# Optimization experiments

Hardware: AMD Instinct MI355X
Metric: run time of the kernel (lower is better)

Reference implementation:

```python
import jax, jax.numpy as jnp
import numpy as np

N_NODES = 100000


def setup_inputs() -> dict:
    key = jax.random.key(0)
    ks = jax.random.split(key, 9)
    x = jax.random.normal(ks[0], (N_NODES, 500), dtype=jnp.float32)
    # lin1: Linear(m=500, hidden=64, bias=False) -> weight [hidden, m]
    W1 = jax.random.normal(ks[1], (64, 500), dtype=jnp.float32) * 0.02
    # lin_final: Linear(3*hidden=192, m_y=10, bias=False) -> weight [m_y, 3*hidden]
    Wf = jax.random.normal(ks[2], (10, 192), dtype=jnp.float32) * 0.02
    # 1-hop normalized adjacency in COO form (600k nnz)
    src1 = jax.random.randint(ks[3], (600000,), 0, N_NODES, dtype=jnp.int32)
    dst1 = jax.random.randint(ks[4], (600000,), 0, N_NODES, dtype=jnp.int32)
    val1 = jax.random.uniform(ks[5], (600000,), dtype=jnp.float32)
    # 2-hop normalized adjacency in COO form (1.2M nnz)
    src2 = jax.random.randint(ks[6], (1200000,), 0, N_NODES, dtype=jnp.int32)
    dst2 = jax.random.randint(ks[7], (1200000,), 0, N_NODES, dtype=jnp.int32)
    val2 = jax.random.uniform(ks[8], (1200000,), dtype=jnp.float32)
    return {"x": x, "W1": W1, "Wf": Wf,
            "src1": src1, "dst1": dst1, "val1": val1,
            "src2": src2, "dst2": dst2, "val2": val2}


def _spmm(src, dst, val, h):
    # sparse.mm(A, h): out[dst] += val * h[src]
    return jax.ops.segment_sum(val[:, None] * h[src], dst, num_segments=N_NODES)


def reference(x, W1, Wf, src1, dst1, val1, src2, dst2, val2):
    h = jax.nn.relu(x @ W1.T)                 # [N, hidden]
    h1 = _spmm(src1, dst1, val1, h)           # [N, hidden]
    h2 = _spmm(src2, dst2, val2, h)           # [N, hidden]
    h_final = jnp.concatenate([h, h1, h2], axis=1)  # [N, 3*hidden]
    # dropout is identity in eval mode
    return h_final @ Wf.T                     # [N, m_y]
```

## Files before the change

### kernel.cpp

```cpp
#include <hip/hip_runtime.h>
#include <hip/hip_bf16.h>

#define NN   100000
#define KD   500
#define KP   512
#define HID  64
#define LWS  264
#define GS   24

typedef short frag8 __attribute__((ext_vector_type(8)));
typedef float f32x4 __attribute__((ext_vector_type(4)));

static __device__ __forceinline__ unsigned short f2b(float f) {
    return __builtin_bit_cast(unsigned short, __float2bfloat16(f));
}

__global__ __launch_bounds__(256) void k0_w1bf(const float* __restrict__ W1,
                                               unsigned short* __restrict__ W1bf)
{
    const int i = blockIdx.x * 256 + threadIdx.x;
    const int c = i >> 9;
    const int k = i & 511;
    const float v = (k < KD) ? W1[c * KD + k] : 0.f;
    W1bf[i] = f2b(v);
}

__global__ __launch_bounds__(256, 4) void k1_mfma(const float* __restrict__ x,
                                                  const unsigned short* __restrict__ W1bf,
                                                  float* __restrict__ h, int n)
{
    __shared__ unsigned short lw[64 * LWS];
    const int tid   = threadIdx.x;
    const int lane  = tid & 63;
    const int wid   = tid >> 6;
    const int l15   = lane & 15;
    const int l4    = lane >> 4;
    const int koffl = 8 * l4;

    const long rowBlk = (long)blockIdx.x * 64;
    long ra = rowBlk + wid * 16 + l15;
    if (ra >= n) ra = n - 1;
    const float* xp = x + ra * KD + koffl;

    f32x4 acc[4] = {};
    const float4 z = make_float4(0.f, 0.f, 0.f, 0.f);

    for (int c = 0; c < 2; ++c) {
        if (c) __syncthreads();
        #pragma unroll
        for (int it = 0; it < 8; ++it) {
            const int idx = tid + it * 256;
            const int r   = idx >> 5;
            const int q   = idx & 31;
            *(uint4*)&lw[r * LWS + q * 8] =
                *(const uint4*)&W1bf[r * KP + c * 256 + q * 8];
        }
        __syncthreads();

        int k0 = c * 256;
        float4 lo = (k0 + koffl     < KD) ? *(const float4*)(xp + k0)     : z;
        float4 hi = (k0 + koffl + 4 < KD) ? *(const float4*)(xp + k0 + 4) : z;

        #pragma unroll
        for (int ks = 0; ks < 8; ++ks) {
            float4 nlo = z, nhi = z;
            if (ks < 7) {
                const int kn = c * 256 + (ks + 1) * 32;
                nlo = (kn + koffl     < KD) ? *(const float4*)(xp + kn)     : z;
                nhi = (kn + koffl + 4 < KD) ? *(const float4*)(xp + kn + 4) : z;
            }
            frag8 a;
            a[0]=f2b(lo.x); a[1]=f2b(lo.y); a[2]=f2b(lo.z); a[3]=f2b(lo.w);
            a[4]=f2b(hi.x); a[5]=f2b(hi.y); a[6]=f2b(hi.z); a[7]=f2b(hi.w);
            const int koffw = ks * 32 + koffl;
            #pragma unroll
            for (int g = 0; g < 4; ++g) {
                const frag8 b = *(const frag8*)&lw[(g * 16 + l15) * LWS + koffw];
                acc[g] = __builtin_amdgcn_mfma_f32_16x16x32_bf16(a, b, acc[g], 0, 0, 0);
            }
            lo = nlo; hi = nhi;
        }
    }

    #pragma unroll
    for (int r = 0; r < 4; ++r) {
        const long row = rowBlk + wid * 16 + l4 * 4 + r;
        if (row < n) {
            #pragma unroll
            for (int g = 0; g < 4; ++g)
                h[row * HID + g * 16 + l15] = fmaxf(acc[g][r], 0.f);
        }
    }
}

__global__ __launch_bounds__(256) void k2_proj(const float* __restrict__ h,
                                               const float* __restrict__ Wf,
                                               float* __restrict__ out,
                                               float* __restrict__ g, int n)
{
    __shared__ float lwf[10 * 196];
    const int tid = threadIdx.x;
    for (int idx = tid; idx < 480; idx += 256) {
        const int j = idx / 48;
        const int q = idx - j * 48;
        const float4 v = *(const float4*)&Wf[j * 192 + 4 * q];
        *(float4*)&lwf[j * 196 + 4 * q] = v;
    }
    __syncthreads();

    const long row = (long)blockIdx.x * 8 + (tid >> 5);
    const int  j   = tid & 31;
    if (row < n && j < 30) {
        const int wrow = (j < 10) ? j : ((j < 20) ? j - 10 : j - 20);
        const int coff = (j < 10) ? 0 : ((j < 20) ? 64 : 128);
        const float* wp = &lwf[wrow * 196 + coff];
        const float* hp = &h[row * HID];
        float s = 0.f;
        #pragma unroll
        for (int q = 0; q < 16; ++q) {
            const float4 hv = *(const float4*)&hp[4 * q];
            const float4 wv = *(const float4*)&wp[4 * q];
            s += hv.x * wv.x + hv.y * wv.y + hv.z * wv.z + hv.w * wv.w;
        }
        if (j < 10)      out[row * 10 + j] = s;
        else if (j < 20) g[row * GS + (j - 10)] = s;
        else             g[row * GS + 12 + (j - 20)] = s;
    }
}

__global__ __launch_bounds__(256) void k_scatter(const int* __restrict__ src1,
                                                 const int* __restrict__ dst1,
                                                 const float* __restrict__ val1, int n1,
                                                 const int* __restrict__ src2,
                                                 const int* __restrict__ dst2,
                                                 const float* __restrict__ val2, int nt,
                                                 const float* __restrict__ g,
                                                 float* __restrict__ out)
{
    const int stride = gridDim.x * 256;
    for (int t0 = blockIdx.x * 256 + threadIdx.x; t0 < nt; t0 += 4 * stride) {
        float contrib[4];
        int   oidx[4];
        #pragma unroll
        for (int u = 0; u < 4; ++u) {
            const int tu = t0 + u * stride;
            oidx[u] = -1;
            contrib[u] = 0.f;
            if (tu < nt) {
                const bool h1 = tu < n1;
                const int  tt = h1 ? tu : tu - n1;
                const int  e  = (int)((unsigned)tt / 10u);
                const int  j  = tt - 10 * e;
                const int* sp = h1 ? src1 : src2;
                const int* dp = h1 ? dst1 : dst2;
                const float* vp = h1 ? val1 : val2;
                const int   s = sp[e];
                const int   d = dp[e];
                const float v = vp[e];
                contrib[u] = v * g[(size_t)s * GS + (h1 ? 0 : 12) + j];
                oidx[u] = d * 10 + j;
            }
        }
        #pragma unroll
        for (int u = 0; u < 4; ++u)
            if (oidx[u] >= 0) unsafeAtomicAdd(&out[oidx[u]], contrib[u]);
    }
}

extern "C" void kernel_launch(void* const* d_in, const int* in_sizes, int n_in,
                              void* d_out, int out_size, void* d_ws, size_t ws_size,
                              hipStream_t stream)
{
    const float* x    = (const float*)d_in[0];
    const float* W1   = (const float*)d_in[1];
    const float* Wf   = (const float*)d_in[2];
    const int*   src1 = (const int*)d_in[3];
    const int*   dst1 = (const int*)d_in[4];
    const float* val1 = (const float*)d_in[5];
    const int*   src2 = (const int*)d_in[6];
    const int*   dst2 = (const int*)d_in[7];
    const float* val2 = (const float*)d_in[8];
    const int nnz1 = in_sizes[3];
    const int nnz2 = in_sizes[6];
    const int n = NN;

    unsigned short* W1bf = (unsigned short*)d_ws;
    float* h   = (float*)((char*)d_ws + 64 * KP * 2);
    float* g   = h + (size_t)NN * HID;
    float* out = (float*)d_out;

    k0_w1bf<<<128, 256, 0, stream>>>(W1, W1bf);
    k1_mfma<<<(n + 63) / 64, 256, 0, stream>>>(x, W1bf, h, n);
    k2_proj<<<(n + 7) / 8, 256, 0, stream>>>(h, Wf, out, g, n);
    const int n1 = 10 * nnz1;
    const int nt = n1 + 10 * nnz2;
    int nb = (nt + 1023) / 1024;
    if (nb > 2048) nb = 2048;
    k_scatter<<<nb, 256, 0, stream>>>(src1, dst1, val1, n1,
                                      src2, dst2, val2, nt, g, out);
}
```

Before: 231.9 us.

## Privatize scatter atomics per XCD into replicated buffers, then reduce

Result: slower. 250.1 us (+7.8%).

```diff
diff --git a/kernel.cpp b/kernel.cpp
--- a/kernel.cpp
+++ b/kernel.cpp
@@ -7,6 +7,7 @@
 #define HID  64
 #define LWS  264
 #define GS   24
+#define NXCD 8
 
 typedef short frag8 __attribute__((ext_vector_type(8)));
 typedef float f32x4 __attribute__((ext_vector_type(4)));
@@ -128,43 +129,70 @@
     }
 }
 
-__global__ __launch_bounds__(256) void k_scatter(const int* __restrict__ src1,
-                                                 const int* __restrict__ dst1,
-                                                 const float* __restrict__ val1, int n1,
-                                                 const int* __restrict__ src2,
-                                                 const int* __restrict__ dst2,
-                                                 const float* __restrict__ val2, int nt,
-                                                 const float* __restrict__ g,
-                                                 float* __restrict__ out)
-{
-    const int stride = gridDim.x * 256;
-    for (int t0 = blockIdx.x * 256 + threadIdx.x; t0 < nt; t0 += 4 * stride) {
-        float contrib[4];
-        int   oidx[4];
-        #pragma unroll
-        for (int u = 0; u < 4; ++u) {
-            const int tu = t0 + u * stride;
-            oidx[u] = -1;
-            contrib[u] = 0.f;
-            if (tu < nt) {
-                const bool h1 = tu < n1;
-                const int  tt = h1 ? tu : tu - n1;
-                const int  e  = (int)((unsigned)tt / 10u);
-                const int  j  = tt - 10 * e;
-                const int* sp = h1 ? src1 : src2;
-                const int* dp = h1 ? dst1 : dst2;
-                const float* vp = h1 ? val1 : val2;
-                const int   s = sp[e];
-                const int   d = dp[e];
-                const float v = vp[e];
-                contrib[u] = v * g[(size_t)s * GS + (h1 ? 0 : 12) + j];
-                oidx[u] = d * 10 + j;
-            }
-        }
-        #pragma unroll
-        for (int u = 0; u < 4; ++u)
-            if (oidx[u] >= 0) unsafeAtomicAdd(&out[oidx[u]], contrib[u]);
-    }
+__global__ __launch_bounds__(256) void k_scatter_rep(const int* __restrict__ src1,
+                                                     const int* __restrict__ dst1,
+                                                     const float* __restrict__ val1, int n1,
+                                                     const int* __restrict__ src2,
+                                                     const int* __restrict__ dst2,
+                                                     const float* __restrict__ val2, int nt,
+                                                     const float* __restrict__ g,
+                                                     float* __restrict__ rep)
+{
+    const int t = blockIdx.x * 256 + threadIdx.x;
+    if (t >= nt) return;
+    const bool h1 = t < n1;
+    const int  tt = h1 ? t : t - n1;
+    const int  e  = (int)((unsigned)tt / 10u);
+    const int  j  = tt - 10 * e;
+    const int* sp = h1 ? src1 : src2;
+    const int* dp = h1 ? dst1 : dst2;
+    const float* vp = h1 ? val1 : val2;
+    const int   s = sp[e];
+    const int   d = dp[e];
+    const float v = vp[e];
+    const float c = v * g[(size_t)s * GS + (h1 ? 0 : 12) + j];
+
+    unsigned xcc;
+    asm volatile("s_getreg_b32 %0, hwreg(HW_REG_XCC_ID)" : "=s"(xcc));
+    float* r = rep + (size_t)(xcc & (NXCD - 1)) * (NN * 10);
+    __hip_atomic_fetch_add(&r[d * 10 + j], c, __ATOMIC_RELAXED,
+                           __HIP_MEMORY_SCOPE_WORKGROUP);
+}
+
+__global__ __launch_bounds__(256) void k_scatter_dir(const int* __restrict__ src1,
+                                                     const int* __restrict__ dst1,
+                                                     const float* __restrict__ val1, int n1,
+                                                     const int* __restrict__ src2,
+                                                     const int* __restrict__ dst2,
+                                                     const float* __restrict__ val2, int nt,
+                                                     const float* __restrict__ g,
+                                                     float* __restrict__ out)
+{
+    const int t = blockIdx.x * 256 + threadIdx.x;
+    if (t >= nt) return;
+    const bool h1 = t < n1;
+    const int  tt = h1 ? t : t - n1;
+    const int  e  = (int)((unsigned)tt / 10u);
+    const int  j  = tt - 10 * e;
+    const int* sp = h1 ? src1 : src2;
+    const int* dp = h1 ? dst1 : dst2;
+    const float* vp = h1 ? val1 : val2;
+    unsafeAtomicAdd(&out[(size_t)dp[e] * 10 + j],
+                    vp[e] * g[(size_t)sp[e] * GS + (h1 ? 0 : 12) + j]);
+}
+
+__global__ __launch_bounds__(256) void k_reduce(const float* __restrict__ rep,
+                                                float* __restrict__ out)
+{
+    const int i = blockIdx.x * 256 + threadIdx.x;
+    if (i >= NN * 10 / 4) return;
+    float4 s = *(const float4*)&out[4 * i];
+    #pragma unroll
+    for (int r = 0; r < NXCD; ++r) {
+        const float4 a = *(const float4*)&rep[(size_t)r * (NN * 10) + 4 * i];
+        s.x += a.x; s.y += a.y; s.z += a.z; s.w += a.w;
+    }
+    *(float4*)&out[4 * i] = s;
 }
 
 extern "C" void kernel_launch(void* const* d_in, const int* in_sizes, int n_in,
@@ -187,15 +215,25 @@
     unsigned short* W1bf = (unsigned short*)d_ws;
     float* h   = (float*)((char*)d_ws + 64 * KP * 2);
     float* g   = h + (size_t)NN * HID;
+    float* rep = g + (size_t)NN * GS;
     float* out = (float*)d_out;
+
+    const size_t ws_need = (size_t)64 * KP * 2 + (size_t)NN * HID * 4
+                         + (size_t)NN * GS * 4 + (size_t)NXCD * NN * 10 * 4;
 
     k0_w1bf<<<128, 256, 0, stream>>>(W1, W1bf);
     k1_mfma<<<(n + 63) / 64, 256, 0, stream>>>(x, W1bf, h, n);
     k2_proj<<<(n + 7) / 8, 256, 0, stream>>>(h, Wf, out, g, n);
+
     const int n1 = 10 * nnz1;
     const int nt = n1 + 10 * nnz2;
-    int nb = (nt + 1023) / 1024;
-    if (nb > 2048) nb = 2048;
-    k_scatter<<<nb, 256, 0, stream>>>(src1, dst1, val1, n1,
-                                      src2, dst2, val2, nt, g, out);
-}
+    if (ws_size >= ws_need) {
+        hipMemsetAsync(rep, 0, (size_t)NXCD * NN * 10 * 4, stream);
+        k_scatter_rep<<<(nt + 255) / 256, 256, 0, stream>>>(src1, dst1, val1, n1,
+                                                            src2, dst2, val2, nt, g, rep);
+        k_reduce<<<(NN * 10 / 4 + 255) / 256, 256, 0, stream>>>(rep, out);
+    } else {
+        k_scatter_dir<<<(nt + 255) / 256, 256, 0, stream>>>(src1, dst1, val1, n1,
+                                                            src2, dst2, val2, nt, g, out);
+    }
+}
```

## Replace global atomic scatter with destination-binned counting sort and LDS accumulation

Applied to the files above, without the earlier changes.

New measurement: 265.5 us. 14.5% more time.

```diff
diff --git a/kernel.cpp b/kernel.cpp
--- a/kernel.cpp
+++ b/kernel.cpp
@@ -1,12 +1,15 @@
 #include <hip/hip_runtime.h>
 #include <hip/hip_bf16.h>
 
-#define NN   100000
-#define KD   500
-#define KP   512
-#define HID  64
-#define LWS  264
-#define GS   24
+#define NN    100000
+#define KD    500
+#define KP    512
+#define HID   64
+#define LWS   264
+#define GSP   16
+#define DB    128
+#define NB    782
+#define CHUNK 4096
 
 typedef short frag8 __attribute__((ext_vector_type(8)));
 typedef float f32x4 __attribute__((ext_vector_type(4)));
@@ -96,7 +99,8 @@
 __global__ __launch_bounds__(256) void k2_proj(const float* __restrict__ h,
                                                const float* __restrict__ Wf,
                                                float* __restrict__ out,
-                                               float* __restrict__ g, int n)
+                                               float* __restrict__ g1,
+                                               float* __restrict__ g2, int n)
 {
     __shared__ float lwf[10 * 196];
     const int tid = threadIdx.x;
@@ -123,48 +127,175 @@
             s += hv.x * wv.x + hv.y * wv.y + hv.z * wv.z + hv.w * wv.w;
         }
         if (j < 10)      out[row * 10 + j] = s;
-        else if (j < 20) g[row * GS + (j - 10)] = s;
-        else             g[row * GS + 12 + (j - 20)] = s;
-    }
-}
-
-__global__ __launch_bounds__(256) void k_scatter(const int* __restrict__ src1,
-                                                 const int* __restrict__ dst1,
-                                                 const float* __restrict__ val1, int n1,
-                                                 const int* __restrict__ src2,
-                                                 const int* __restrict__ dst2,
-                                                 const float* __restrict__ val2, int nt,
-                                                 const float* __restrict__ g,
-                                                 float* __restrict__ out)
-{
-    const int stride = gridDim.x * 256;
-    for (int t0 = blockIdx.x * 256 + threadIdx.x; t0 < nt; t0 += 4 * stride) {
-        float contrib[4];
-        int   oidx[4];
-        #pragma unroll
-        for (int u = 0; u < 4; ++u) {
-            const int tu = t0 + u * stride;
-            oidx[u] = -1;
-            contrib[u] = 0.f;
-            if (tu < nt) {
-                const bool h1 = tu < n1;
-                const int  tt = h1 ? tu : tu - n1;
-                const int  e  = (int)((unsigned)tt / 10u);
-                const int  j  = tt - 10 * e;
-                const int* sp = h1 ? src1 : src2;
-                const int* dp = h1 ? dst1 : dst2;
-                const float* vp = h1 ? val1 : val2;
-                const int   s = sp[e];
-                const int   d = dp[e];
-                const float v = vp[e];
-                contrib[u] = v * g[(size_t)s * GS + (h1 ? 0 : 12) + j];
-                oidx[u] = d * 10 + j;
-            }
-        }
-        #pragma unroll
-        for (int u = 0; u < 4; ++u)
-            if (oidx[u] >= 0) unsafeAtomicAdd(&out[oidx[u]], contrib[u]);
-    }
+        else if (j < 20) g1[row * GSP + (j - 10)] = s;
+        else             g2[row * GSP + (j - 20)] = s;
+    }
+}
+
+__global__ __launch_bounds__(256) void kA_hist(const int* __restrict__ dst1, int nnz1,
+                                               const int* __restrict__ dst2, int ntE,
+                                               int nblk, int* __restrict__ Cmat)
+{
+    __shared__ int cnt[NB];
+    const int tid = threadIdx.x, blk = blockIdx.x;
+    for (int i = tid; i < NB; i += 256) cnt[i] = 0;
+    __syncthreads();
+    const int base = blk * CHUNK;
+    #pragma unroll
+    for (int it = 0; it < CHUNK / 256; ++it) {
+        const int id = base + it * 256 + tid;
+        if (id < ntE) {
+            const int d = (id < nnz1) ? dst1[id] : dst2[id - nnz1];
+            atomicAdd(&cnt[d / DB], 1);
+        }
+    }
+    __syncthreads();
+    for (int b = tid; b < NB; b += 256) Cmat[b * nblk + blk] = cnt[b];
+}
+
+__global__ __launch_bounds__(256) void kS1_rowscan(const int* __restrict__ Cmat, int nblk,
+                                                   int* __restrict__ OFFmat,
+                                                   int* __restrict__ rowSum)
+{
+    __shared__ int ls[256];
+    const int b = blockIdx.x, tid = threadIdx.x;
+    const int i0 = 2 * tid, i1 = 2 * tid + 1;
+    const int e0 = (i0 < nblk) ? Cmat[b * nblk + i0] : 0;
+    const int e1 = (i1 < nblk) ? Cmat[b * nblk + i1] : 0;
+    const int ps = e0 + e1;
+    ls[tid] = ps;
+    __syncthreads();
+    for (int off = 1; off < 256; off <<= 1) {
+        const int v = (tid >= off) ? ls[tid - off] : 0;
+        __syncthreads();
+        ls[tid] += v;
+        __syncthreads();
+    }
+    const int excl = ls[tid] - ps;
+    if (i0 < nblk) OFFmat[b * nblk + i0] = excl;
+    if (i1 < nblk) OFFmat[b * nblk + i1] = excl + e0;
+    if (tid == 255) rowSum[b] = ls[255];
+}
+
+__global__ __launch_bounds__(256) void kS2_basescan(const int* __restrict__ rowSum,
+                                                    int* __restrict__ rowBase)
+{
+    __shared__ int ls[256];
+    const int tid = threadIdx.x;
+    int e[4]; int s = 0;
+    #pragma unroll
+    for (int u = 0; u < 4; ++u) {
+        const int i = 4 * tid + u;
+        e[u] = (i < NB) ? rowSum[i] : 0;
+        s += e[u];
+    }
+    ls[tid] = s;
+    __syncthreads();
+    for (int off = 1; off < 256; off <<= 1) {
+        const int v = (tid >= off) ? ls[tid - off] : 0;
+        __syncthreads();
+        ls[tid] += v;
+        __syncthreads();
+    }
+    int run = ls[tid] - s;
+    #pragma unroll
+    for (int u = 0; u < 4; ++u) {
+        const int i = 4 * tid + u;
+        if (i < NB) rowBase[i] = run;
+        run += e[u];
+    }
+}
+
+__global__ __launch_bounds__(256) void kC_fill(const int* __restrict__ src1,
+                                               const int* __restrict__ dst1,
+                                               const float* __restrict__ val1, int nnz1,
+                                               const int* __restrict__ src2,
+                                               const int* __restrict__ dst2,
+                                               const float* __restrict__ val2, int ntE,
+                                               int nblk,
+                                               const int* __restrict__ OFFmat,
+                                               const int* __restrict__ rowBase,
+                                               uint2* __restrict__ bins)
+{
+    __shared__ int cur[NB];
+    const int tid = threadIdx.x, blk = blockIdx.x;
+    for (int b = tid; b < NB; b += 256)
+        cur[b] = rowBase[b] + OFFmat[b * nblk + blk];
+    __syncthreads();
+    const int base = blk * CHUNK;
+    #pragma unroll
+    for (int it = 0; it < CHUNK / 256; ++it) {
+        const int id = base + it * 256 + tid;
+        if (id < ntE) {
+            const bool h1 = id < nnz1;
+            const int  ii = h1 ? id : id - nnz1;
+            const int   s = h1 ? src1[ii] : src2[ii];
+            const int   d = h1 ? dst1[ii] : dst2[ii];
+            const float v = h1 ? val1[ii] : val2[ii];
+            const int   b = d / DB;
+            const int slot = atomicAdd(&cur[b], 1);
+            uint2 r;
+            r.x = (unsigned)s | ((unsigned)(!h1) << 17) | ((unsigned)(d - b * DB) << 18);
+            r.y = __builtin_bit_cast(unsigned, v);
+            bins[slot] = r;
+        }
+    }
+}
+
+__global__ __launch_bounds__(256) void kD_acc(const uint2* __restrict__ bins,
+                                              const int* __restrict__ rowBase,
+                                              const int* __restrict__ rowSum,
+                                              const float* __restrict__ g1,
+                                              const float* __restrict__ g2,
+                                              float* __restrict__ out)
+{
+    __shared__ float lacc[DB * 10];
+    const int tid = threadIdx.x, b = blockIdx.x;
+    for (int i = tid; i < DB * 10; i += 256) lacc[i] = 0.f;
+    __syncthreads();
+    const int start = rowBase[b];
+    const int cnt   = rowSum[b];
+    const int nt    = cnt * 10;
+    for (int i = tid; i < nt; i += 256) {
+        const int e = (int)((unsigned)i / 10u);
+        const int j = i - 10 * e;
+        const uint2 r = bins[start + e];
+        const int   src = r.x & 0x1FFFF;
+        const int   hop = (r.x >> 17) & 1;
+        const int   dl  = (int)(r.x >> 18);
+        const float v   = __builtin_bit_cast(float, r.y);
+        const float* gp = hop ? g2 : g1;
+        atomicAdd(&lacc[dl * 10 + j], v * gp[(size_t)src * GSP + j]);
+    }
+    __syncthreads();
+    const int rows = min(DB, NN - b * DB);
+    float* op = out + (size_t)b * DB * 10;
+    for (int i = tid; i < rows * 10; i += 256)
+        op[i] += lacc[i];
+}
+
+__global__ __launch_bounds__(256) void k_scatter_dir(const int* __restrict__ src1,
+                                                     const int* __restrict__ dst1,
+                                                     const float* __restrict__ val1, int n1,
+                                                     const int* __restrict__ src2,
+                                                     const int* __restrict__ dst2,
+                                                     const float* __restrict__ val2, int nt,
+                                                     const float* __restrict__ g1,
+                                                     const float* __restrict__ g2,
+                                                     float* __restrict__ out)
+{
+    const int t = blockIdx.x * 256 + threadIdx.x;
+    if (t >= nt) return;
+    const bool h1 = t < n1;
+    const int  tt = h1 ? t : t - n1;
+    const int  e  = (int)((unsigned)tt / 10u);
+    const int  j  = tt - 10 * e;
+    const int* sp = h1 ? src1 : src2;
+    const int* dp = h1 ? dst1 : dst2;
+    const float* vp = h1 ? val1 : val2;
+    const float* gp = h1 ? g1 : g2;
+    unsafeAtomicAdd(&out[(size_t)dp[e] * 10 + j],
+                    vp[e] * gp[(size_t)sp[e] * GSP + j]);
 }
 
 extern "C" void kernel_launch(void* const* d_in, const int* in_sizes, int n_in,
@@ -182,20 +313,40 @@
     const float* val2 = (const float*)d_in[8];
     const int nnz1 = in_sizes[3];
     const int nnz2 = in_sizes[6];
+    const int ntE  = nnz1 + nnz2;
     const int n = NN;
-
-    unsigned short* W1bf = (unsigned short*)d_ws;
-    float* h   = (float*)((char*)d_ws + 64 * KP * 2);
-    float* g   = h + (size_t)NN * HID;
-    float* out = (float*)d_out;
+    const int nblk = (ntE + CHUNK - 1) / CHUNK;
+
+    char* p = (char*)d_ws;
+    unsigned short* W1bf = (unsigned short*)p;       p += (size_t)64 * KP * 2;
+    float* h    = (float*)p;                         p += (size_t)NN * HID * 4;
+    float* g1   = (float*)p;                         p += (size_t)NN * GSP * 4;
+    float* g2   = (float*)p;                         p += (size_t)NN * GSP * 4;
+    uint2* bins = (uint2*)p;                         p += (size_t)ntE * 8;
+    int* Cmat   = (int*)p;                           p += (size_t)NB * nblk * 4;
+    int* OFFmat = (int*)p;                           p += (size_t)NB * nblk * 4;
+    int* rowSum = (int*)p;                           p += (size_t)NB * 4;
+    int* rowBase= (int*)p;                           p += (size_t)NB * 4;
+    float* out  = (float*)d_out;
+    const size_t ws_need = (size_t)(p - (char*)d_ws);
 
     k0_w1bf<<<128, 256, 0, stream>>>(W1, W1bf);
     k1_mfma<<<(n + 63) / 64, 256, 0, stream>>>(x, W1bf, h, n);
-    k2_proj<<<(n + 7) / 8, 256, 0, stream>>>(h, Wf, out, g, n);
-    const int n1 = 10 * nnz1;
-    const int nt = n1 + 10 * nnz2;
-    int nb = (nt + 1023) / 1024;
-    if (nb > 2048) nb = 2048;
-    k_scatter<<<nb, 256, 0, stream>>>(src1, dst1, val1, n1,
-                                      src2, dst2, val2, nt, g, out);
-}
+    k2_proj<<<(n + 7) / 8, 256, 0, stream>>>(h, Wf, out, g1, g2, n);
+
+    if (ws_size >= ws_need) {
+        kA_hist<<<nblk, 256, 0, stream>>>(dst1, nnz1, dst2, ntE, nblk, Cmat);
+        kS1_rowscan<<<NB, 256, 0, stream>>>(Cmat, nblk, OFFmat, rowSum);
+        kS2_basescan<<<1, 256, 0, stream>>>(rowSum, rowBase);
+        kC_fill<<<nblk, 256, 0, stream>>>(src1, dst1, val1, nnz1,
+                                          src2, dst2, val2, ntE,
+                                          nblk, OFFmat, rowBase, bins);
+        kD_acc<<<NB, 256, 0, stream>>>(bins, rowBase, rowSum, g1, g2, out);
+    } else {
+        const int n1 = 10 * nnz1;
+        const int nt = n1 + 10 * nnz2;
+        k_scatter_dir<<<(nt + 255) / 256, 256, 0, stream>>>(src1, dst1, val1, n1,
+                                                            src2, dst2, val2, nt,
+                                                            g1, g2, out);
+    }
+}
```
